# Performance work log

Hardware: AMD Instinct MI355X
Metric: run time of the kernel (lower is better)

The kernel has to match this reference:

```python
import jax, jax.numpy as jnp
import numpy as np

NUM_TRANSFORMS = 8


def _mlp(h, W1, b1, W2, b2, W3, b3):
    h = jax.nn.relu(h @ W1 + b1)
    h = jax.nn.relu(h @ W2 + b2)
    return h @ W3 + b3


def _transforms(x, intensity):
    # x: (B,L,C), intensity: (B,K). Returns stacked (K,B,L,C).
    def t(j):
        return intensity[:, j][:, None, None]  # (B,1,1)
    outs = [
        x,                                  # 0 identity
        x * (1.0 + t(1)),                   # 1 magnitude scale up
        x + t(2),                           # 2 additive shift
        x * (1.0 - t(3)),                   # 3 magnitude scale down
        jnp.tanh(x * (1.0 + t(4))),         # 4 saturating warp
        x * jnp.exp(-t(5)),                 # 5 exponential damping
        x + t(6) * jnp.sin(x),              # 6 nonlinear perturbation
        jnp.flip(x, axis=1) + 0.0 * t(7),   # 7 time reversal
    ]
    return jnp.stack(outs, axis=0)


def setup_inputs() -> dict:
    key = jax.random.key(0)
    ks = jax.random.split(key, 16)
    B, L, C = 64, 2048, 64
    K, F, H = NUM_TRANSFORMS, 24, 64
    D = F + K  # mlp input dim = 32
    x = jax.random.normal(ks[0], (B, L, C), dtype=jnp.float32)
    prev_prob = jax.nn.softmax(jax.random.normal(ks[1], (B, K), dtype=jnp.float32), axis=-1)
    features = jax.random.normal(ks[2], (B, F), dtype=jnp.float32)
    u = jax.random.uniform(ks[3], (B, K), dtype=jnp.float32, minval=1e-6, maxval=1.0 - 1e-6)
    gumbel_noise = -jnp.log(-jnp.log(u))
    s = 0.1
    p = {
        'pW1': jax.random.normal(ks[4], (D, H)) * s, 'pb1': jnp.zeros((H,)),
        'pW2': jax.random.normal(ks[5], (H, H)) * s, 'pb2': jnp.zeros((H,)),
        'pW3': jax.random.normal(ks[6], (H, K)) * s, 'pb3': jnp.zeros((K,)),
        'iW1': jax.random.normal(ks[7], (D, H)) * s, 'ib1': jnp.zeros((H,)),
        'iW2': jax.random.normal(ks[8], (H, H)) * s, 'ib2': jnp.zeros((H,)),
        'iW3': jax.random.normal(ks[9], (H, K)) * s, 'ib3': jnp.zeros((K,)),
    }
    return dict(x=x, prev_prob=prev_prob, features=features, gumbel_noise=gumbel_noise,
                log_temperature=jnp.asarray(0.0, dtype=jnp.float32), **p)


def reference(x, prev_prob, features, gumbel_noise, log_temperature,
              pW1, pb1, pW2, pb2, pW3, pb3,
              iW1, ib1, iW2, ib2, iW3, ib3):
    K = NUM_TRANSFORMS
    mlp_in = jnp.concatenate([prev_prob, features], axis=1)  # (B, K+F)
    prob_logits = _mlp(mlp_in, pW1, pb1, pW2, pb2, pW3, pb3)           # (B,K)
    intensity = jax.nn.softplus(_mlp(mlp_in, iW1, ib1, iW2, ib2, iW3, ib3))  # (B,K)
    prob = jax.nn.softmax(prob_logits, axis=-1)
    tau = jnp.clip(jnp.exp(log_temperature), 0.01, 10.0)
    # gumbel-softmax, hard=True with straight-through estimator (training path)
    y_soft = jax.nn.softmax((prob_logits + gumbel_noise) / tau, axis=-1)
    idx = jnp.argmax(y_soft, axis=-1)
    y_hard = jax.nn.one_hot(idx, K, dtype=y_soft.dtype)
    selection = y_hard + y_soft - jax.lax.stop_gradient(y_soft)  # (B,K)
    selected_idx = jnp.argmax(selection, axis=-1)
    # compute-all-then-mask combine (dense training path _apply_mixed)
    results = _transforms(x, intensity)                 # (K,B,L,C)
    x_aug = jnp.einsum('kblc,bk->blc', results, selection)
    return x_aug, prob, intensity, selected_idx
```

## Files before the change

### kernel.cpp

```cpp
#include <hip/hip_runtime.h>

#define B_  64
#define L_  2048
#define C_  64
#define K_  8
#define F_  24
#define D_  32
#define H_  64

#define XAUG_N   (B_ * L_ * C_)
#define PROB_OFF (XAUG_N)
#define INT_OFF  (PROB_OFF + B_ * K_)
#define SEL_OFF  (INT_OFF + B_ * K_)

#define VEC_PER_BATCH   (L_ * C_ / 4)
#define BLOCKS_PER_B    16
#define VEC_PER_BLOCK   (VEC_PER_BATCH / BLOCKS_PER_B)
#define ITERS           (VEC_PER_BLOCK / 256)

__device__ __forceinline__ float softplus_f(float v) {
    return fmaxf(v, 0.f) + log1pf(expf(-fabsf(v)));
}

__global__ void __launch_bounds__(256) fused_kernel(
    const float* __restrict__ x,
    const float* __restrict__ prev_prob, const float* __restrict__ features,
    const float* __restrict__ gumbel,    const float* __restrict__ log_temp,
    const float* __restrict__ pW1, const float* __restrict__ pb1,
    const float* __restrict__ pW2, const float* __restrict__ pb2,
    const float* __restrict__ pW3, const float* __restrict__ pb3,
    const float* __restrict__ iW1, const float* __restrict__ ib1,
    const float* __restrict__ iW2, const float* __restrict__ ib2,
    const float* __restrict__ iW3, const float* __restrict__ ib3,
    float* __restrict__ out)
{
    const int b   = blockIdx.x >> 4;
    const int blk = blockIdx.x & (BLOCKS_PER_B - 1);
    const int tid = threadIdx.x;

    __shared__ float s_in[D_];
    __shared__ float s_a[H_];
    __shared__ float s_b[H_];
    __shared__ float s_log[2 * K_];
    __shared__ float s_desc[4];

    const int h = tid;

    if (tid < D_) s_in[tid] = (tid < K_) ? prev_prob[b * K_ + tid]
                                         : features[b * F_ + (tid - K_)];
    __syncthreads();

    if (tid < H_) {
        float acc = pb1[h];
        #pragma unroll
        for (int d = 0; d < D_; ++d) acc = fmaf(s_in[d], pW1[d * H_ + h], acc);
        s_a[h] = fmaxf(acc, 0.f);
    }
    __syncthreads();

    if (tid < H_) {
        float acc = pb2[h];
        #pragma unroll
        for (int d = 0; d < H_; ++d) acc = fmaf(s_a[d], pW2[d * H_ + h], acc);
        s_b[h] = fmaxf(acc, 0.f);
    }
    __syncthreads();

    if (tid < K_) {
        float acc = pb3[h];
        #pragma unroll
        for (int d = 0; d < H_; ++d) acc = fmaf(s_b[d], pW3[d * K_ + h], acc);
        s_log[h] = acc;
    }
    __syncthreads();

    if (tid < H_) {
        float acc = ib1[h];
        #pragma unroll
        for (int d = 0; d < D_; ++d) acc = fmaf(s_in[d], iW1[d * H_ + h], acc);
        s_a[h] = fmaxf(acc, 0.f);
    }
    __syncthreads();

    if (tid < H_) {
        float acc = ib2[h];
        #pragma unroll
        for (int d = 0; d < H_; ++d) acc = fmaf(s_a[d], iW2[d * H_ + h], acc);
        s_b[h] = fmaxf(acc, 0.f);
    }
    __syncthreads();

    if (tid < K_) {
        float acc = ib3[h];
        #pragma unroll
        for (int d = 0; d < H_; ++d) acc = fmaf(s_b[d], iW3[d * K_ + h], acc);
        s_log[K_ + h] = acc;
    }
    __syncthreads();

    if (tid == 0) {
        float plog[K_], ilog[K_];
        #pragma unroll
        for (int k = 0; k < K_; ++k) { plog[k] = s_log[k]; ilog[k] = s_log[K_ + k]; }

        float m = plog[0];
        #pragma unroll
        for (int k = 1; k < K_; ++k) m = fmaxf(m, plog[k]);
        float e[K_], se = 0.f;
        #pragma unroll
        for (int k = 0; k < K_; ++k) { e[k] = expf(plog[k] - m); se += e[k]; }

        float inten[K_];
        #pragma unroll
        for (int k = 0; k < K_; ++k) inten[k] = softplus_f(ilog[k]);

        float tau = expf(log_temp[0]);
        tau = fminf(fmaxf(tau, 0.01f), 10.0f);
        float z[K_], m2 = -3.4e38f;
        #pragma unroll
        for (int k = 0; k < K_; ++k) {
            z[k] = (plog[k] + gumbel[b * K_ + k]) / tau;
            m2 = fmaxf(m2, z[k]);
        }
        float se2 = 0.f;
        #pragma unroll
        for (int k = 0; k < K_; ++k) { z[k] = expf(z[k] - m2); se2 += z[k]; }
        int idx = 0; float best = z[0];
        #pragma unroll
        for (int k = 1; k < K_; ++k) { if (z[k] > best) { best = z[k]; idx = k; } }

        float ys  = best / se2;
        float sel = (1.0f + ys) - ys;

        if (blk == 0) {
            #pragma unroll
            for (int k = 0; k < K_; ++k) out[PROB_OFF + b * K_ + k] = e[k] / se;
            #pragma unroll
            for (int k = 0; k < K_; ++k) out[INT_OFF + b * K_ + k] = inten[k];
            out[SEL_OFF + b] = (float)idx;
        }

        const float t = inten[idx];
        int kind; float p0, p1 = 0.f;
        switch (idx) {
            case 0: kind = 0; p0 = sel;                  break;
            case 1: kind = 0; p0 = sel * (1.f + t);      break;
            case 2: kind = 0; p0 = sel; p1 = sel * t;    break;
            case 3: kind = 0; p0 = sel * (1.f - t);      break;
            case 4: kind = 1; p0 = sel; p1 = 1.f + t;    break;
            case 5: kind = 0; p0 = sel * expf(-t);       break;
            case 6: kind = 2; p0 = sel; p1 = sel * t;    break;
            default: kind = 3; p0 = sel;                 break;
        }
        s_desc[0] = (float)kind; s_desc[1] = p0; s_desc[2] = p1;
    }
    __syncthreads();

    int kind = (int)s_desc[0];
    kind = kind < 0 ? 0 : (kind > 3 ? 3 : kind);
    const float p0 = s_desc[1];
    const float p1 = s_desc[2];

    const int base = blk * VEC_PER_BLOCK + tid;
    const float4* xb = (const float4*)x + (size_t)b * VEC_PER_BATCH;
    float4*       ob = (float4*)out + (size_t)b * VEC_PER_BATCH;

    float4 xv[ITERS];
    if (kind == 3) {
        #pragma unroll
        for (int i = 0; i < ITERS; ++i) {
            const int v = base + i * 256;
            const int l = v >> 4, c = v & 15;
            xv[i] = xb[(L_ - 1 - l) * 16 + c];
        }
    } else {
        #pragma unroll
        for (int i = 0; i < ITERS; ++i) xv[i] = xb[base + i * 256];
    }

    if (kind == 0) {
        #pragma unroll
        for (int i = 0; i < ITERS; ++i) {
            float4 r;
            r.x = fmaf(p0, xv[i].x, p1);
            r.y = fmaf(p0, xv[i].y, p1);
            r.z = fmaf(p0, xv[i].z, p1);
            r.w = fmaf(p0, xv[i].w, p1);
            ob[base + i * 256] = r;
        }
    } else if (kind == 1) {
        #pragma unroll
        for (int i = 0; i < ITERS; ++i) {
            float4 r;
            r.x = p0 * tanhf(p1 * xv[i].x);
            r.y = p0 * tanhf(p1 * xv[i].y);
            r.z = p0 * tanhf(p1 * xv[i].z);
            r.w = p0 * tanhf(p1 * xv[i].w);
            ob[base + i * 256] = r;
        }
    } else if (kind == 2) {
        #pragma unroll
        for (int i = 0; i < ITERS; ++i) {
            float4 r;
            r.x = fmaf(p0, xv[i].x, p1 * sinf(xv[i].x));
            r.y = fmaf(p0, xv[i].y, p1 * sinf(xv[i].y));
            r.z = fmaf(p0, xv[i].z, p1 * sinf(xv[i].z));
            r.w = fmaf(p0, xv[i].w, p1 * sinf(xv[i].w));
            ob[base + i * 256] = r;
        }
    } else {
        #pragma unroll
        for (int i = 0; i < ITERS; ++i) {
            float4 r;
            r.x = p0 * xv[i].x; r.y = p0 * xv[i].y;
            r.z = p0 * xv[i].z; r.w = p0 * xv[i].w;
            ob[base + i * 256] = r;
        }
    }
}

extern "C" void kernel_launch(void* const* d_in, const int* in_sizes, int n_in,
                              void* d_out, int out_size, void* d_ws, size_t ws_size,
                              hipStream_t stream) {
    const float* x         = (const float*)d_in[0];
    const float* prev_prob = (const float*)d_in[1];
    const float* features  = (const float*)d_in[2];
    const float* gumbel    = (const float*)d_in[3];
    const float* log_temp  = (const float*)d_in[4];
    const float* pW1 = (const float*)d_in[5];
    const float* pb1 = (const float*)d_in[6];
    const float* pW2 = (const float*)d_in[7];
    const float* pb2 = (const float*)d_in[8];
    const float* pW3 = (const float*)d_in[9];
    const float* pb3 = (const float*)d_in[10];
    const float* iW1 = (const float*)d_in[11];
    const float* ib1 = (const float*)d_in[12];
    const float* iW2 = (const float*)d_in[13];
    const float* ib2 = (const float*)d_in[14];
    const float* iW3 = (const float*)d_in[15];
    const float* ib3 = (const float*)d_in[16];

    float* out = (float*)d_out;

    hipLaunchKernelGGL(fused_kernel, dim3(B_ * BLOCKS_PER_B), dim3(256), 0, stream,
                       x, prev_prob, features, gumbel, log_temp,
                       pW1, pb1, pW2, pb2, pW3, pb3,
                       iW1, ib1, iW2, ib2, iW3, ib3,
                       out);
}
```

Measured before the change: 126.4 us.

## Run MLPs per wave with shuffles and overlap x loads with gating

Two waves of each block now compute the probability and intensity MLPs in parallel, passing activations with wave shuffles instead of shared memory and syncthreads. The other waves issue their x loads immediately, so the loads overlap the MLP work. Every thread then redundantly computes the selection and transform parameters after a single barrier. Time reversal is handled by reading x in forward order and writing the output reversed, so the loads no longer depend on the selected transform. This trades extra per-thread scalar work and register pressure (launch bounds now request 4 blocks) for fewer barriers and less serialisation before the memory stream starts.

```diff
diff --git a/kernel.cpp b/kernel.cpp
--- a/kernel.cpp
+++ b/kernel.cpp
@@ -22,7 +22,37 @@
     return fmaxf(v, 0.f) + log1pf(expf(-fabsf(v)));
 }
 
-__global__ void __launch_bounds__(256) fused_kernel(
+__device__ __forceinline__ void wave_mlp(
+    int lane, const float* in_v,
+    const float* __restrict__ W1, const float* __restrict__ b1,
+    const float* __restrict__ W2, const float* __restrict__ b2,
+    const float* __restrict__ W3, const float* __restrict__ b3,
+    float* out8)
+{
+    float acc = b1[lane];
+    #pragma unroll
+    for (int d = 0; d < D_; ++d) acc = fmaf(in_v[d], W1[d * H_ + lane], acc);
+    const float a1 = fmaxf(acc, 0.f);
+
+    acc = b2[lane];
+    #pragma unroll
+    for (int d = 0; d < H_; ++d) acc = fmaf(__shfl(a1, d), W2[d * H_ + lane], acc);
+    const float a2 = fmaxf(acc, 0.f);
+
+    const float4 w3a = *(const float4*)(W3 + lane * K_);
+    const float4 w3b = *(const float4*)(W3 + lane * K_ + 4);
+    float pr[K_] = { a2 * w3a.x, a2 * w3a.y, a2 * w3a.z, a2 * w3a.w,
+                     a2 * w3b.x, a2 * w3b.y, a2 * w3b.z, a2 * w3b.w };
+    #pragma unroll
+    for (int k = 0; k < K_; ++k) {
+        float p = pr[k];
+        #pragma unroll
+        for (int off = 32; off > 0; off >>= 1) p += __shfl_xor(p, off);
+        out8[k] = p + b3[k];
+    }
+}
+
+__global__ void __launch_bounds__(256, 4) fused_kernel(
     const float* __restrict__ x,
     const float* __restrict__ prev_prob, const float* __restrict__ features,
     const float* __restrict__ gumbel,    const float* __restrict__ log_temp,
@@ -34,148 +64,102 @@
     const float* __restrict__ iW3, const float* __restrict__ ib3,
     float* __restrict__ out)
 {
-    const int b   = blockIdx.x >> 4;
-    const int blk = blockIdx.x & (BLOCKS_PER_B - 1);
-    const int tid = threadIdx.x;
-
-    __shared__ float s_in[D_];
-    __shared__ float s_a[H_];
-    __shared__ float s_b[H_];
+    const int b    = blockIdx.x >> 4;
+    const int blk  = blockIdx.x & (BLOCKS_PER_B - 1);
+    const int tid  = threadIdx.x;
+    const int wave = tid >> 6;
+    const int lane = tid & 63;
+
     __shared__ float s_log[2 * K_];
-    __shared__ float s_desc[4];
-
-    const int h = tid;
-
-    if (tid < D_) s_in[tid] = (tid < K_) ? prev_prob[b * K_ + tid]
-                                         : features[b * F_ + (tid - K_)];
-    __syncthreads();
-
-    if (tid < H_) {
-        float acc = pb1[h];
-        #pragma unroll
-        for (int d = 0; d < D_; ++d) acc = fmaf(s_in[d], pW1[d * H_ + h], acc);
-        s_a[h] = fmaxf(acc, 0.f);
-    }
-    __syncthreads();
-
-    if (tid < H_) {
-        float acc = pb2[h];
-        #pragma unroll
-        for (int d = 0; d < H_; ++d) acc = fmaf(s_a[d], pW2[d * H_ + h], acc);
-        s_b[h] = fmaxf(acc, 0.f);
-    }
-    __syncthreads();
-
-    if (tid < K_) {
-        float acc = pb3[h];
-        #pragma unroll
-        for (int d = 0; d < H_; ++d) acc = fmaf(s_b[d], pW3[d * K_ + h], acc);
-        s_log[h] = acc;
-    }
-    __syncthreads();
-
-    if (tid < H_) {
-        float acc = ib1[h];
-        #pragma unroll
-        for (int d = 0; d < D_; ++d) acc = fmaf(s_in[d], iW1[d * H_ + h], acc);
-        s_a[h] = fmaxf(acc, 0.f);
-    }
-    __syncthreads();
-
-    if (tid < H_) {
-        float acc = ib2[h];
-        #pragma unroll
-        for (int d = 0; d < H_; ++d) acc = fmaf(s_a[d], iW2[d * H_ + h], acc);
-        s_b[h] = fmaxf(acc, 0.f);
-    }
-    __syncthreads();
-
-    if (tid < K_) {
-        float acc = ib3[h];
-        #pragma unroll
-        for (int d = 0; d < H_; ++d) acc = fmaf(s_b[d], iW3[d * K_ + h], acc);
-        s_log[K_ + h] = acc;
-    }
-    __syncthreads();
-
-    if (tid == 0) {
-        float plog[K_], ilog[K_];
-        #pragma unroll
-        for (int k = 0; k < K_; ++k) { plog[k] = s_log[k]; ilog[k] = s_log[K_ + k]; }
-
-        float m = plog[0];
-        #pragma unroll
-        for (int k = 1; k < K_; ++k) m = fmaxf(m, plog[k]);
-        float e[K_], se = 0.f;
-        #pragma unroll
-        for (int k = 0; k < K_; ++k) { e[k] = expf(plog[k] - m); se += e[k]; }
-
-        float inten[K_];
-        #pragma unroll
-        for (int k = 0; k < K_; ++k) inten[k] = softplus_f(ilog[k]);
-
-        float tau = expf(log_temp[0]);
-        tau = fminf(fmaxf(tau, 0.01f), 10.0f);
-        float z[K_], m2 = -3.4e38f;
-        #pragma unroll
-        for (int k = 0; k < K_; ++k) {
-            z[k] = (plog[k] + gumbel[b * K_ + k]) / tau;
-            m2 = fmaxf(m2, z[k]);
-        }
-        float se2 = 0.f;
-        #pragma unroll
-        for (int k = 0; k < K_; ++k) { z[k] = expf(z[k] - m2); se2 += z[k]; }
-        int idx = 0; float best = z[0];
-        #pragma unroll
-        for (int k = 1; k < K_; ++k) { if (z[k] > best) { best = z[k]; idx = k; } }
-
-        float ys  = best / se2;
-        float sel = (1.0f + ys) - ys;
-
-        if (blk == 0) {
-            #pragma unroll
-            for (int k = 0; k < K_; ++k) out[PROB_OFF + b * K_ + k] = e[k] / se;
-            #pragma unroll
-            for (int k = 0; k < K_; ++k) out[INT_OFF + b * K_ + k] = inten[k];
-            out[SEL_OFF + b] = (float)idx;
-        }
-
-        const float t = inten[idx];
-        int kind; float p0, p1 = 0.f;
-        switch (idx) {
-            case 0: kind = 0; p0 = sel;                  break;
-            case 1: kind = 0; p0 = sel * (1.f + t);      break;
-            case 2: kind = 0; p0 = sel; p1 = sel * t;    break;
-            case 3: kind = 0; p0 = sel * (1.f - t);      break;
-            case 4: kind = 1; p0 = sel; p1 = 1.f + t;    break;
-            case 5: kind = 0; p0 = sel * expf(-t);       break;
-            case 6: kind = 2; p0 = sel; p1 = sel * t;    break;
-            default: kind = 3; p0 = sel;                 break;
-        }
-        s_desc[0] = (float)kind; s_desc[1] = p0; s_desc[2] = p1;
-    }
-    __syncthreads();
-
-    int kind = (int)s_desc[0];
-    kind = kind < 0 ? 0 : (kind > 3 ? 3 : kind);
-    const float p0 = s_desc[1];
-    const float p1 = s_desc[2];
 
     const int base = blk * VEC_PER_BLOCK + tid;
     const float4* xb = (const float4*)x + (size_t)b * VEC_PER_BATCH;
     float4*       ob = (float4*)out + (size_t)b * VEC_PER_BATCH;
 
     float4 xv[ITERS];
-    if (kind == 3) {
-        #pragma unroll
-        for (int i = 0; i < ITERS; ++i) {
-            const int v = base + i * 256;
-            const int l = v >> 4, c = v & 15;
-            xv[i] = xb[(L_ - 1 - l) * 16 + c];
-        }
+    if (wave >= 2) {
+        #pragma unroll
+        for (int i = 0; i < ITERS; ++i) xv[i] = xb[base + i * 256];
     } else {
+        float in_v[D_];
+        #pragma unroll
+        for (int d = 0; d < K_; ++d) in_v[d] = prev_prob[b * K_ + d];
+        #pragma unroll
+        for (int d = 0; d < F_; ++d) in_v[K_ + d] = features[b * F_ + d];
+
+        const bool w0 = (wave == 0);
+        float lg[K_];
+        wave_mlp(lane, in_v,
+                 w0 ? pW1 : iW1, w0 ? pb1 : ib1,
+                 w0 ? pW2 : iW2, w0 ? pb2 : ib2,
+                 w0 ? pW3 : iW3, w0 ? pb3 : ib3, lg);
+
+        if (lane == 0) {
+            #pragma unroll
+            for (int k = 0; k < K_; ++k) s_log[wave * K_ + k] = lg[k];
+        }
+        __builtin_amdgcn_sched_barrier(0);
         #pragma unroll
         for (int i = 0; i < ITERS; ++i) xv[i] = xb[base + i * 256];
+    }
+
+    __syncthreads();
+
+    float plog[K_], ilog[K_];
+    #pragma unroll
+    for (int k = 0; k < K_; ++k) { plog[k] = s_log[k]; ilog[k] = s_log[K_ + k]; }
+
+    float m = plog[0];
+    #pragma unroll
+    for (int k = 1; k < K_; ++k) m = fmaxf(m, plog[k]);
+    float e[K_], se = 0.f;
+    #pragma unroll
+    for (int k = 0; k < K_; ++k) { e[k] = expf(plog[k] - m); se += e[k]; }
+
+    float inten[K_];
+    #pragma unroll
+    for (int k = 0; k < K_; ++k) inten[k] = softplus_f(ilog[k]);
+
+    float tau = expf(log_temp[0]);
+    tau = fminf(fmaxf(tau, 0.01f), 10.0f);
+    float z[K_], m2 = -3.4e38f;
+    #pragma unroll
+    for (int k = 0; k < K_; ++k) {
+        z[k] = (plog[k] + gumbel[b * K_ + k]) / tau;
+        m2 = fmaxf(m2, z[k]);
+    }
+    float se2 = 0.f;
+    #pragma unroll
+    for (int k = 0; k < K_; ++k) { z[k] = expf(z[k] - m2); se2 += z[k]; }
+    int idx = 0; float best = z[0];
+    #pragma unroll
+    for (int k = 1; k < K_; ++k) { if (z[k] > best) { best = z[k]; idx = k; } }
+
+    const float ys  = best / se2;
+    const float sel = (1.0f + ys) - ys;
+
+    if (blk == 0 && tid == 0) {
+        #pragma unroll
+        for (int k = 0; k < K_; ++k) out[PROB_OFF + b * K_ + k] = e[k] / se;
+        #pragma unroll
+        for (int k = 0; k < K_; ++k) out[INT_OFF + b * K_ + k] = inten[k];
+        out[SEL_OFF + b] = (float)idx;
+    }
+
+    float t = inten[0];
+    #pragma unroll
+    for (int k = 1; k < K_; ++k) t = (idx == k) ? inten[k] : t;
+
+    int kind; float p0, p1 = 0.f;
+    switch (idx) {
+        case 0: kind = 0; p0 = sel;                  break;
+        case 1: kind = 0; p0 = sel * (1.f + t);      break;
+        case 2: kind = 0; p0 = sel; p1 = sel * t;    break;
+        case 3: kind = 0; p0 = sel * (1.f - t);      break;
+        case 4: kind = 1; p0 = sel; p1 = 1.f + t;    break;
+        case 5: kind = 0; p0 = sel * expf(-t);       break;
+        case 6: kind = 2; p0 = sel; p1 = sel * t;    break;
+        default: kind = 3; p0 = sel;                 break;
     }
 
     if (kind == 0) {
@@ -211,10 +195,12 @@
     } else {
         #pragma unroll
         for (int i = 0; i < ITERS; ++i) {
+            const int v = base + i * 256;
+            const int l = v >> 4, c = v & 15;
             float4 r;
             r.x = p0 * xv[i].x; r.y = p0 * xv[i].y;
             r.z = p0 * xv[i].z; r.w = p0 * xv[i].w;
-            ob[base + i * 256] = r;
+            ob[(L_ - 1 - l) * 16 + c] = r;
         }
     }
 }
```

New measurement: 125.4 us. No clear change (-0.8%).
